# Kernel optimization log

Measured on AMD Instinct MI355X. Metric: run time of the kernel, lower is better.

The kernel has to match this reference:

```python
import jax, jax.numpy as jnp
import numpy as np

B, L, D = 16, 128, 128
VOCAB = 30000
OUT = 10


def setup_inputs() -> dict:
    key = jax.random.key(0)
    ks = jax.random.split(key, 16)
    s = 0.02
    inp = {
        "word_data": jax.random.randint(ks[0], (B, L), 0, VOCAB, dtype=jnp.int32),
        "position_data": jnp.tile(jnp.arange(L, dtype=jnp.int32)[None, :], (B, 1)),
        "sentence_length": jax.random.randint(ks[1], (B,), 1, L + 1, dtype=jnp.int32),
        # parameters
        "word_emb": jax.random.normal(ks[2], (VOCAB + 1, D), jnp.float32) * s,
        "pos_emb": jax.random.normal(ks[3], (L, D), jnp.float32) * s,
        # dw1/du1 act on the tiled last axis (D copies of e) => weight shape (D*D, D)
        "W_dw1": jax.random.normal(ks[4], (D * D, D), jnp.float32) * s,
        "b_dw1": jnp.zeros((D,), jnp.float32),
        "W_dw2": jax.random.normal(ks[5], (D, D), jnp.float32) * s,
        "b_dw2": jnp.zeros((D,), jnp.float32),
        "W_du1": jax.random.normal(ks[6], (D * D, D), jnp.float32) * s,
        "b_du1": jnp.zeros((D,), jnp.float32),
        "W_du2": jax.random.normal(ks[7], (D, D), jnp.float32) * s,
        "b_du2": jnp.zeros((D,), jnp.float32),
        "W_d4": jax.random.normal(ks[8], (D, D), jnp.float32) * s,
        "b_d4": jnp.zeros((D,), jnp.float32),
        "W_d5": jax.random.normal(ks[9], (L * D, OUT), jnp.float32) * s,
    }
    return inp


def reference(word_data, position_data, sentence_length,
              word_emb, pos_emb,
              W_dw1, b_dw1, W_dw2, b_dw2,
              W_du1, b_du1, W_du2, b_du2,
              W_d4, b_d4, W_d5):
    d = word_emb.shape[-1]
    e = word_emb[word_data] + pos_emb[position_data]          # (B, L, D)

    # tf.tile(..., [1,1,L,D]) makes word_embedding1[b,i,j,:] = D concatenated
    # copies of e[b,i].  Dense(W, b) on that concat == e @ (sum of the D
    # (D,D) row-blocks of W) + b, independent of j.  Exact same math,
    # without materializing the (B,L,L,D*D) tensor.
    W_dw1_eff = W_dw1.reshape(d, d, d).sum(axis=0)            # (D, D)
    W_du1_eff = W_du1.reshape(d, d, d).sum(axis=0)            # (D, D)

    p = e @ W_dw1_eff + b_dw1                                 # dw1(tiled)  (B,L,D), row term
    q = e @ W_dw2 + b_dw2                                     # dw2(e)      (B,L,D), col term
    # S[b,i,j,:] = p[b,i] + q[b,j]

    # du2 is affine: du2(S) = p@W_du2 + q@W_du2 + b_du2 (split row/col)
    r = (e @ W_du1_eff + b_du1) + p @ W_du2                   # row part (B,L,D)
    s = q @ W_du2 + b_du2                                     # col part (B,L,D)

    weight = jnp.tanh(r[:, :, None, :] + s[:, None, :, :])    # (B,L,L,D)
    S = p[:, :, None, :] + q[:, None, :, :]                   # (B,L,L,D)
    sent = jnp.sum(weight * S, axis=2)                        # (B,L,D)

    h = jax.nn.relu(sent @ W_d4 + b_d4)                       # Dropout inactive at inference
    out = h.reshape(h.shape[0], -1) @ W_d5                    # (B, OUT), no bias
    return out
```

## Files before the change

### kernel.cpp

```cpp
#include <hip/hip_runtime.h>
#include <hip/hip_bf16.h>


#define LOG2E2 2.8853900817779268f

__global__ __launch_bounds__(1024) void k1_eff(const float* __restrict__ Wdw1,
                                               const float* __restrict__ Wdu1,
                                               float* __restrict__ Weff,
                                               float* __restrict__ out) {
    __shared__ float red[8][128];
    int m = blockIdx.x >> 7;
    int j = blockIdx.x & 127;
    int g = threadIdx.x >> 7;
    int k = threadIdx.x & 127;
    const float* src = (m ? Wdu1 : Wdw1) + (size_t)g * 16 * 16384 + j * 128 + k;
    float acc = 0.f;
    #pragma unroll
    for (int i = 0; i < 16; ++i)
        acc += src[(size_t)i * 16384];
    red[g][k] = acc;
    if (blockIdx.x == 0 && threadIdx.x < 160) out[threadIdx.x] = 0.f;
    __syncthreads();
    if (g == 0) {
        float s = 0.f;
        #pragma unroll
        for (int t = 0; t < 8; ++t) s += red[t][k];
        Weff[m * 16384 + j * 128 + k] = s;
    }
}

__global__ __launch_bounds__(256) void k2_w4(const float* __restrict__ Weff,
                                             const float* __restrict__ Wdw2,
                                             const float* __restrict__ Wdu2,
                                             const float* __restrict__ bdw1,
                                             const float* __restrict__ bdw2,
                                             const float* __restrict__ bdu1,
                                             const float* __restrict__ bdu2,
                                             float* __restrict__ W4,
                                             float* __restrict__ bias4) {
    __shared__ float w1row[128], w2row[128];
    int j = blockIdx.x;
    int c = threadIdx.x & 127;
    int which = threadIdx.x >> 7;
    if (which == 0) w1row[c] = Weff[j * 128 + c];
    else            w2row[c] = Wdw2[j * 128 + c];
    __syncthreads();
    const float* srow = which ? w2row : w1row;
    float acc = which ? 0.f : Weff[16384 + j * 128 + c];
    #pragma unroll 4
    for (int k = 0; k < 128; ++k)
        acc += srow[k] * Wdu2[k * 128 + c];
    if (which == 0) {
        W4[j * 512 + c]       = w1row[c];
        W4[j * 512 + 256 + c] = acc;
    } else {
        W4[j * 512 + 128 + c] = w2row[c];
        W4[j * 512 + 384 + c] = acc;
    }
    if (j == 0) {
        const float* bsrc = which ? bdw2 : bdw1;
        float bacc = which ? bdu2[c] : bdu1[c];
        for (int k = 0; k < 128; ++k)
            bacc += bsrc[k] * Wdu2[k * 128 + c];
        if (which == 0) { bias4[c] = bdw1[c];       bias4[256 + c] = bacc; }
        else            { bias4[128 + c] = bdw2[c]; bias4[384 + c] = bacc; }
    }
}

__global__ __launch_bounds__(512) void k3_pqrs(const int* __restrict__ word,
                                               const int* __restrict__ pos,
                                               const float* __restrict__ wemb,
                                               const float* __restrict__ pemb,
                                               const float* __restrict__ W4,
                                               const float* __restrict__ bias4,
                                               float* __restrict__ pqrs) {
    __shared__ float eT[128][8];
    int b = blockIdx.x >> 4;
    int l0 = (blockIdx.x & 15) << 3;
    for (int idx = threadIdx.x; idx < 1024; idx += 512) {
        int ll = idx >> 7, d = idx & 127;
        int l = l0 + ll;
        int wid = word[b * 128 + l];
        int pid = pos[b * 128 + l];
        eT[d][ll] = wemb[wid * 128 + d] + pemb[pid * 128 + d];
    }
    __syncthreads();
    int c = threadIdx.x;
    float acc[8] = {0,0,0,0,0,0,0,0};
    for (int d = 0; d < 128; ++d) {
        float w = W4[d * 512 + c];
        float4 e0 = *(const float4*)&eT[d][0];
        float4 e1 = *(const float4*)&eT[d][4];
        acc[0] += e0.x * w; acc[1] += e0.y * w;
        acc[2] += e0.z * w; acc[3] += e0.w * w;
        acc[4] += e1.x * w; acc[5] += e1.y * w;
        acc[6] += e1.z * w; acc[7] += e1.w * w;
    }
    float bv = bias4[c];
    #pragma unroll
    for (int ll = 0; ll < 8; ++ll)
        pqrs[(b * 128 + l0 + ll) * 512 + c] = acc[ll] + bv;
}

__global__ __launch_bounds__(256) void k4_sent(const float* __restrict__ pqrs,
                                               float* __restrict__ sent) {
    __shared__ float2 qe[128][8];
    int b  = blockIdx.x >> 5;
    int i0 = ((blockIdx.x >> 4) & 1) << 6;
    int d0 = (blockIdx.x & 15) << 3;
    for (int idx = threadIdx.x; idx < 2048; idx += 256) {
        int which = idx >> 10;
        int j = (idx >> 3) & 127;
        int dl = idx & 7;
        float v = pqrs[(b * 128 + j) * 512 + (which ? 384 : 128) + d0 + dl];
        if (which) qe[j][dl].y = __builtin_amdgcn_exp2f(v * LOG2E2);
        else       qe[j][dl].x = v;
    }
    __syncthreads();
    int dl = threadIdx.x & 7;
    int ii = threadIdx.x >> 3;
    int iA = i0 + ii, iB = i0 + ii + 32;
    int baseA = (b * 128 + iA) * 512 + d0 + dl;
    int baseB = (b * 128 + iB) * 512 + d0 + dl;
    float pA = pqrs[baseA];
    float pB = pqrs[baseB];
    float ErA = __builtin_amdgcn_exp2f(pqrs[baseA + 256] * LOG2E2);
    float ErB = __builtin_amdgcn_exp2f(pqrs[baseB + 256] * LOG2E2);
    float accA = 0.f, accB = 0.f;
    #pragma unroll 8
    for (int j = 0; j < 128; ++j) {
        float2 v = qe[j][dl];
        float tA = fmaf(ErA, v.y, 1.f);
        float tB = fmaf(ErB, v.y, 1.f);
        float gA = __builtin_amdgcn_rcpf(tA);
        float gB = __builtin_amdgcn_rcpf(tB);
        float uA = pA + v.x;
        float uB = pB + v.x;
        float thA = fmaf(-2.f, gA, 1.f);
        float thB = fmaf(-2.f, gB, 1.f);
        accA = fmaf(thA, uA, accA);
        accB = fmaf(thB, uB, accB);
    }
    sent[(b * 128 + iA) * 128 + d0 + dl] = accA;
    sent[(b * 128 + iB) * 128 + d0 + dl] = accB;
}

__global__ __launch_bounds__(512) void k5_out(const float* __restrict__ sent,
                                              const float* __restrict__ Wd4,
                                              const float* __restrict__ bd4,
                                              const float* __restrict__ Wd5,
                                              float* __restrict__ out) {
    __shared__ float eT[128][8];
    int b = blockIdx.x >> 4;
    int l0 = (blockIdx.x & 15) << 3;
    for (int idx = threadIdx.x; idx < 1024; idx += 512) {
        int ll = idx >> 7, d = idx & 127;
        eT[d][ll] = sent[(b * 128 + l0 + ll) * 128 + d];
    }
    __syncthreads();
    int c = threadIdx.x & 127;
    int q = threadIdx.x >> 7;
    float a0 = 0.f, a1 = 0.f;
    #pragma unroll 4
    for (int d = 0; d < 128; ++d) {
        float w = Wd4[d * 128 + c];
        float2 e = *(const float2*)&eT[d][q * 2];
        a0 += e.x * w;
        a1 += e.y * w;
    }
    float bv = bd4[c];
    a0 = fmaxf(a0 + bv, 0.f);
    a1 = fmaxf(a1 + bv, 0.f);
    int lA = l0 + q * 2, lB = lA + 1;
    const float* w5a = Wd5 + ((size_t)(lA * 128 + c)) * 10;
    const float* w5b = Wd5 + ((size_t)(lB * 128 + c)) * 10;
    float acc[10];
    #pragma unroll
    for (int o = 0; o < 10; ++o)
        acc[o] = a0 * w5a[o] + a1 * w5b[o];
    #pragma unroll
    for (int o = 0; o < 10; ++o)
        #pragma unroll
        for (int s = 32; s > 0; s >>= 1)
            acc[o] += __shfl_down(acc[o], s, 64);
    __shared__ float wred[8][10];
    int lane = threadIdx.x & 63, w = threadIdx.x >> 6;
    if (lane == 0) {
        #pragma unroll
        for (int o = 0; o < 10; ++o) wred[w][o] = acc[o];
    }
    __syncthreads();
    if (threadIdx.x < 10) {
        float v = 0.f;
        #pragma unroll
        for (int ww = 0; ww < 8; ++ww) v += wred[ww][threadIdx.x];
        atomicAdd(&out[b * 10 + threadIdx.x], v);
    }
}

extern "C" void kernel_launch(void* const* d_in, const int* in_sizes, int n_in,
                              void* d_out, int out_size, void* d_ws, size_t ws_size,
                              hipStream_t stream) {
    const int*   word = (const int*)d_in[0];
    const int*   pos  = (const int*)d_in[1];
    const float* wemb = (const float*)d_in[3];
    const float* pemb = (const float*)d_in[4];
    const float* Wdw1 = (const float*)d_in[5];
    const float* bdw1 = (const float*)d_in[6];
    const float* Wdw2 = (const float*)d_in[7];
    const float* bdw2 = (const float*)d_in[8];
    const float* Wdu1 = (const float*)d_in[9];
    const float* bdu1 = (const float*)d_in[10];
    const float* Wdu2 = (const float*)d_in[11];
    const float* bdu2 = (const float*)d_in[12];
    const float* Wd4  = (const float*)d_in[13];
    const float* bd4  = (const float*)d_in[14];
    const float* Wd5  = (const float*)d_in[15];

    float* ws    = (float*)d_ws;
    float* Weff  = ws;
    float* W4    = ws + 32768;
    float* bias4 = ws + 98304;
    float* pqrs  = ws + 98816;
    float* sent  = ws + 1147392;
    float* out   = (float*)d_out;

    k1_eff <<<256, 1024, 0, stream>>>(Wdw1, Wdu1, Weff, out);
    k2_w4  <<<128,  256, 0, stream>>>(Weff, Wdw2, Wdu2, bdw1, bdw2, bdu1, bdu2, W4, bias4);
    k3_pqrs<<<256,  512, 0, stream>>>(word, pos, wemb, pemb, W4, bias4, pqrs);
    k4_sent<<<512,  256, 0, stream>>>(pqrs, sent);
    k5_out <<<256,  512, 0, stream>>>(sent, Wd4, bd4, Wd5, out);
}
```

Baseline: 55.36 us.

## Fuse weight-prep kernels and simplify tanh accumulation via column-sum identity

Merges the Weff reduction and W4 construction into one kernel, removing a launch and the Weff round trip through global memory. The du1 term and the p@Wdu2 term become separate W4 columns (640 wide), and k4 adds them before the exponent. The inner loop drops one FMA per element by using tanh = 1 - 2*sigmoid-like g: it accumulates u*g and recovers the sum as 128*p + sum(q) - 2*acc, with a per-block column sum of q. The cost is a wider k3 output (more pqrs traffic and more k3 work) and an extra reduction and barrier in k4.

```diff
diff --git a/kernel.cpp b/kernel.cpp
--- a/kernel.cpp
+++ b/kernel.cpp
@@ -4,70 +4,96 @@
 
 #define LOG2E2 2.8853900817779268f
 
-__global__ __launch_bounds__(1024) void k1_eff(const float* __restrict__ Wdw1,
+__global__ __launch_bounds__(1024) void k12_w4(const float* __restrict__ Wdw1,
                                                const float* __restrict__ Wdu1,
-                                               float* __restrict__ Weff,
+                                               const float* __restrict__ Wdw2,
+                                               const float* __restrict__ Wdu2,
+                                               const float* __restrict__ bdw1,
+                                               const float* __restrict__ bdw2,
+                                               const float* __restrict__ bdu1,
+                                               const float* __restrict__ bdu2,
+                                               float* __restrict__ W4,
+                                               float* __restrict__ bias4,
                                                float* __restrict__ out) {
     __shared__ float red[8][128];
-    int m = blockIdx.x >> 7;
-    int j = blockIdx.x & 127;
+    __shared__ float srow[128];
+    int j = blockIdx.x >> 1;
+    int m = blockIdx.x & 1;
     int g = threadIdx.x >> 7;
     int k = threadIdx.x & 127;
+
     const float* src = (m ? Wdu1 : Wdw1) + (size_t)g * 16 * 16384 + j * 128 + k;
     float acc = 0.f;
     #pragma unroll
     for (int i = 0; i < 16; ++i)
         acc += src[(size_t)i * 16384];
     red[g][k] = acc;
-    if (blockIdx.x == 0 && threadIdx.x < 160) out[threadIdx.x] = 0.f;
+    if (blockIdx.x == 2 && threadIdx.x < 160) out[threadIdx.x] = 0.f;
     __syncthreads();
     if (g == 0) {
         float s = 0.f;
         #pragma unroll
         for (int t = 0; t < 8; ++t) s += red[t][k];
-        Weff[m * 16384 + j * 128 + k] = s;
-    }
-}
-
-__global__ __launch_bounds__(256) void k2_w4(const float* __restrict__ Weff,
-                                             const float* __restrict__ Wdw2,
-                                             const float* __restrict__ Wdu2,
-                                             const float* __restrict__ bdw1,
-                                             const float* __restrict__ bdw2,
-                                             const float* __restrict__ bdu1,
-                                             const float* __restrict__ bdu2,
-                                             float* __restrict__ W4,
-                                             float* __restrict__ bias4) {
-    __shared__ float w1row[128], w2row[128];
-    int j = blockIdx.x;
-    int c = threadIdx.x & 127;
-    int which = threadIdx.x >> 7;
-    if (which == 0) w1row[c] = Weff[j * 128 + c];
-    else            w2row[c] = Wdw2[j * 128 + c];
-    __syncthreads();
-    const float* srow = which ? w2row : w1row;
-    float acc = which ? 0.f : Weff[16384 + j * 128 + c];
-    #pragma unroll 4
-    for (int k = 0; k < 128; ++k)
-        acc += srow[k] * Wdu2[k * 128 + c];
-    if (which == 0) {
-        W4[j * 512 + c]       = w1row[c];
-        W4[j * 512 + 256 + c] = acc;
-    } else {
-        W4[j * 512 + 128 + c] = w2row[c];
-        W4[j * 512 + 384 + c] = acc;
-    }
+        W4[j * 640 + (m ? 256 : 0) + k] = s;
+        if (m == 0) {
+            srow[k] = s;
+        } else {
+            float w2 = Wdw2[j * 128 + k];
+            srow[k] = w2;
+            W4[j * 640 + 128 + k] = w2;
+        }
+    }
+    __syncthreads();
+
+    {
+        int kq = threadIdx.x >> 7;
+        int c  = threadIdx.x & 127;
+        float a = 0.f;
+        #pragma unroll
+        for (int t = 0; t < 16; ++t) {
+            int kk = kq * 16 + t;
+            a += srow[kk] * Wdu2[kk * 128 + c];
+        }
+        red[kq][c] = a;
+        __syncthreads();
+        if (kq == 0) {
+            float tot = 0.f;
+            #pragma unroll
+            for (int t = 0; t < 8; ++t) tot += red[t][c];
+            W4[j * 640 + (m ? 512 : 384) + c] = tot;
+        }
+    }
+
     if (j == 0) {
-        const float* bsrc = which ? bdw2 : bdw1;
-        float bacc = which ? bdu2[c] : bdu1[c];
-        for (int k = 0; k < 128; ++k)
-            bacc += bsrc[k] * Wdu2[k * 128 + c];
-        if (which == 0) { bias4[c] = bdw1[c];       bias4[256 + c] = bacc; }
-        else            { bias4[128 + c] = bdw2[c]; bias4[384 + c] = bacc; }
-    }
-}
-
-__global__ __launch_bounds__(512) void k3_pqrs(const int* __restrict__ word,
+        __syncthreads();
+        int kq = threadIdx.x >> 7;
+        int c  = threadIdx.x & 127;
+        const float* bsrc = m ? bdw2 : bdw1;
+        float a = 0.f;
+        #pragma unroll
+        for (int t = 0; t < 16; ++t) {
+            int kk = kq * 16 + t;
+            a += bsrc[kk] * Wdu2[kk * 128 + c];
+        }
+        red[kq][c] = a;
+        __syncthreads();
+        if (kq == 0) {
+            float tot = 0.f;
+            #pragma unroll
+            for (int t = 0; t < 8; ++t) tot += red[t][c];
+            if (m == 0) {
+                bias4[c]       = bdw1[c];
+                bias4[384 + c] = tot;
+            } else {
+                bias4[128 + c] = bdw2[c];
+                bias4[256 + c] = bdu1[c];
+                bias4[512 + c] = bdu2[c] + tot;
+            }
+        }
+    }
+}
+
+__global__ __launch_bounds__(640) void k3_pqrs(const int* __restrict__ word,
                                                const int* __restrict__ pos,
                                                const float* __restrict__ wemb,
                                                const float* __restrict__ pemb,
@@ -77,7 +103,7 @@
     __shared__ float eT[128][8];
     int b = blockIdx.x >> 4;
     int l0 = (blockIdx.x & 15) << 3;
-    for (int idx = threadIdx.x; idx < 1024; idx += 512) {
+    for (int idx = threadIdx.x; idx < 1024; idx += 640) {
         int ll = idx >> 7, d = idx & 127;
         int l = l0 + ll;
         int wid = word[b * 128 + l];
@@ -88,7 +114,7 @@
     int c = threadIdx.x;
     float acc[8] = {0,0,0,0,0,0,0,0};
     for (int d = 0; d < 128; ++d) {
-        float w = W4[d * 512 + c];
+        float w = W4[d * 640 + c];
         float4 e0 = *(const float4*)&eT[d][0];
         float4 e1 = *(const float4*)&eT[d][4];
         acc[0] += e0.x * w; acc[1] += e0.y * w;
@@ -99,33 +125,47 @@
     float bv = bias4[c];
     #pragma unroll
     for (int ll = 0; ll < 8; ++ll)
-        pqrs[(b * 128 + l0 + ll) * 512 + c] = acc[ll] + bv;
+        pqrs[(size_t)(b * 128 + l0 + ll) * 640 + c] = acc[ll] + bv;
 }
 
 __global__ __launch_bounds__(256) void k4_sent(const float* __restrict__ pqrs,
                                                float* __restrict__ sent) {
     __shared__ float2 qe[128][8];
+    __shared__ float SqL[8];
     int b  = blockIdx.x >> 5;
-    int i0 = ((blockIdx.x >> 4) & 1) << 6;
+    int ih = (blockIdx.x >> 4) & 1;
     int d0 = (blockIdx.x & 15) << 3;
     for (int idx = threadIdx.x; idx < 2048; idx += 256) {
         int which = idx >> 10;
         int j = (idx >> 3) & 127;
         int dl = idx & 7;
-        float v = pqrs[(b * 128 + j) * 512 + (which ? 384 : 128) + d0 + dl];
+        float v = pqrs[(size_t)(b * 128 + j) * 640 + (which ? 512 : 128) + d0 + dl];
         if (which) qe[j][dl].y = __builtin_amdgcn_exp2f(v * LOG2E2);
         else       qe[j][dl].x = v;
     }
     __syncthreads();
+    if (threadIdx.x < 64) {
+        int dl = threadIdx.x >> 3;
+        int g  = threadIdx.x & 7;
+        float s = 0.f;
+        #pragma unroll
+        for (int t = 0; t < 16; ++t) s += qe[g * 16 + t][dl].x;
+        s += __shfl_xor(s, 1, 64);
+        s += __shfl_xor(s, 2, 64);
+        s += __shfl_xor(s, 4, 64);
+        if (g == 0) SqL[dl] = s;
+    }
+    __syncthreads();
+
     int dl = threadIdx.x & 7;
     int ii = threadIdx.x >> 3;
-    int iA = i0 + ii, iB = i0 + ii + 32;
-    int baseA = (b * 128 + iA) * 512 + d0 + dl;
-    int baseB = (b * 128 + iB) * 512 + d0 + dl;
+    int iA = ih * 64 + ii, iB = iA + 32;
+    size_t baseA = (size_t)(b * 128 + iA) * 640 + d0 + dl;
+    size_t baseB = (size_t)(b * 128 + iB) * 640 + d0 + dl;
     float pA = pqrs[baseA];
     float pB = pqrs[baseB];
-    float ErA = __builtin_amdgcn_exp2f(pqrs[baseA + 256] * LOG2E2);
-    float ErB = __builtin_amdgcn_exp2f(pqrs[baseB + 256] * LOG2E2);
+    float ErA = __builtin_amdgcn_exp2f((pqrs[baseA + 256] + pqrs[baseA + 384]) * LOG2E2);
+    float ErB = __builtin_amdgcn_exp2f((pqrs[baseB + 256] + pqrs[baseB + 384]) * LOG2E2);
     float accA = 0.f, accB = 0.f;
     #pragma unroll 8
     for (int j = 0; j < 128; ++j) {
@@ -136,13 +176,12 @@
         float gB = __builtin_amdgcn_rcpf(tB);
         float uA = pA + v.x;
         float uB = pB + v.x;
-        float thA = fmaf(-2.f, gA, 1.f);
-        float thB = fmaf(-2.f, gB, 1.f);
-        accA = fmaf(thA, uA, accA);
-        accB = fmaf(thB, uB, accB);
-    }
-    sent[(b * 128 + iA) * 128 + d0 + dl] = accA;
-    sent[(b * 128 + iB) * 128 + d0 + dl] = accB;
+        accA = fmaf(uA, gA, accA);
+        accB = fmaf(uB, gB, accB);
+    }
+    float Sq = SqL[dl];
+    sent[(b * 128 + iA) * 128 + d0 + dl] = fmaf(-2.f, accA, fmaf(128.f, pA, Sq));
+    sent[(b * 128 + iB) * 128 + d0 + dl] = fmaf(-2.f, accB, fmaf(128.f, pB, Sq));
 }
 
 __global__ __launch_bounds__(512) void k5_out(const float* __restrict__ sent,
@@ -218,16 +257,15 @@
     const float* Wd5  = (const float*)d_in[15];
 
     float* ws    = (float*)d_ws;
-    float* Weff  = ws;
-    float* W4    = ws + 32768;
-    float* bias4 = ws + 98304;
-    float* pqrs  = ws + 98816;
-    float* sent  = ws + 1147392;
+    float* W4    = ws;
+    float* bias4 = ws + 81920;
+    float* pqrs  = ws + 82560;
+    float* sent  = ws + 1393280;
     float* out   = (float*)d_out;
 
-    k1_eff <<<256, 1024, 0, stream>>>(Wdw1, Wdu1, Weff, out);
-    k2_w4  <<<128,  256, 0, stream>>>(Weff, Wdw2, Wdu2, bdw1, bdw2, bdu1, bdu2, W4, bias4);
-    k3_pqrs<<<256,  512, 0, stream>>>(word, pos, wemb, pemb, W4, bias4, pqrs);
+    k12_w4 <<<256, 1024, 0, stream>>>(Wdw1, Wdu1, Wdw2, Wdu2,
+                                      bdw1, bdw2, bdu1, bdu2, W4, bias4, out);
+    k3_pqrs<<<256,  640, 0, stream>>>(word, pos, wemb, pemb, W4, bias4, pqrs);
     k4_sent<<<512,  256, 0, stream>>>(pqrs, sent);
     k5_out <<<256,  512, 0, stream>>>(sent, Wd4, bd4, Wd5, out);
 }
```

Result: faster. 45.65 us (-17.5%).
